# Optimization experiments

Measured on AMD Instinct MI355X. Metric: run time of the kernel, lower is better.

The kernel has to match this reference:

```python
import jax, jax.numpy as jnp
import numpy as np

DIM = 256
NUM_HEADS = 8
HEAD_DIM = DIM // NUM_HEADS  # 32 (MQA: k/v projected to a single head)
RPE_DIM = 128
P = 10            # cpb table resolution per axis ('bilinear_4_10')
MAX_VALUE = 4.0
LOG_SCALE = 512.0
LOG2_8 = 3.0      # np.log2(8)


def _trilinear_sample(table, grid):
    """torch F.grid_sample 3D, mode='bilinear', padding_mode='zeros', align_corners=True.
    table: [C, D, H, W]; grid: [M, 3] with (x,y,z) in [-1,1] -> returns [C, M]."""
    C, D, H, W = table.shape
    x = (grid[:, 0] + 1.0) * 0.5 * (W - 1)
    y = (grid[:, 1] + 1.0) * 0.5 * (H - 1)
    z = (grid[:, 2] + 1.0) * 0.5 * (D - 1)
    x0f, y0f, z0f = jnp.floor(x), jnp.floor(y), jnp.floor(z)
    wx1, wy1, wz1 = x - x0f, y - y0f, z - z0f
    wx0, wy0, wz0 = 1.0 - wx1, 1.0 - wy1, 1.0 - wz1
    x0 = x0f.astype(jnp.int32); x1 = x0 + 1
    y0 = y0f.astype(jnp.int32); y1 = y0 + 1
    z0 = z0f.astype(jnp.int32); z1 = z0 + 1

    def corner(iz, iy, ix, w):
        inb = (iz >= 0) & (iz < D) & (iy >= 0) & (iy < H) & (ix >= 0) & (ix < W)
        v = table[:, jnp.clip(iz, 0, D - 1), jnp.clip(iy, 0, H - 1), jnp.clip(ix, 0, W - 1)]
        return v * jnp.where(inb, w, 0.0)[None, :]

    return (corner(z0, y0, x0, wz0 * wy0 * wx0) + corner(z0, y0, x1, wz0 * wy0 * wx1)
          + corner(z0, y1, x0, wz0 * wy1 * wx0) + corner(z0, y1, x1, wz0 * wy1 * wx1)
          + corner(z1, y0, x0, wz1 * wy0 * wx0) + corner(z1, y0, x1, wz1 * wy0 * wx1)
          + corner(z1, y1, x0, wz1 * wy1 * wx0) + corner(z1, y1, x1, wz1 * wy1 * wx1))


def setup_inputs() -> dict:
    rng = jax.random.key(0)
    ks = jax.random.split(rng, 12)
    B, nQ, nK = 2, 256, 2048
    s = 0.02
    return {
        "query": jax.random.normal(ks[0], (nQ, B, DIM), jnp.float32),
        "key": jax.random.normal(ks[1], (nK, B, DIM), jnp.float32),
        "reference_point": jax.random.normal(ks[2], (B, nQ, 8, 3), jnp.float32),
        "reference_angle": jax.random.normal(ks[3], (B, nQ), jnp.float32),
        "xyz_vol": jax.random.normal(ks[4], (B, nK, 3), jnp.float32),
        "q_w": jax.random.normal(ks[5], (DIM, DIM), jnp.float32) * s,
        "q_b": jnp.zeros((DIM,), jnp.float32),
        "k_w": jax.random.normal(ks[6], (DIM, HEAD_DIM), jnp.float32) * s,
        "k_b": jnp.zeros((HEAD_DIM,), jnp.float32),
        "v_w": jax.random.normal(ks[7], (DIM, HEAD_DIM), jnp.float32) * s,
        "v_b": jnp.zeros((HEAD_DIM,), jnp.float32),
        "proj_w": jax.random.normal(ks[8], (DIM, DIM), jnp.float32) * s,
        "proj_b": jnp.zeros((DIM,), jnp.float32),
        "cpb_w1": jax.random.normal(ks[9], (8, 3, RPE_DIM), jnp.float32) * s,
        "cpb_b1": jnp.zeros((8, RPE_DIM), jnp.float32),
        "cpb_w2": jax.random.normal(ks[10], (8, RPE_DIM, NUM_HEADS), jnp.float32) * s,
    }


def reference(query, key, reference_point, reference_angle, xyz_vol,
              q_w, q_b, k_w, k_b, v_w, v_b, proj_w, proj_b,
              cpb_w1, cpb_b1, cpb_w2):
    B, nQ = reference_point.shape[:2]
    nK = xyz_vol.shape[1]
    q_in = jnp.transpose(query, (1, 0, 2))  # [B, nQ, DIM]
    k_in = jnp.transpose(key, (1, 0, 2))    # [B, nK, DIM]

    # CPB MLP evaluated on the fixed coords table -> per-corner tables [8, NUM_HEADS, P, P, P]
    lin = jnp.linspace(-MAX_VALUE, MAX_VALUE, P, dtype=jnp.float32)
    coords = jnp.stack(jnp.meshgrid(lin, lin, lin, indexing='ij'), axis=-1)  # [P,P,P,3]
    hid = jax.nn.relu(jnp.einsum('pqrc,icd->ipqrd', coords, cpb_w1) + cpb_b1[:, None, None, None, :])
    tables = jnp.einsum('ipqrd,idh->ihpqr', hid, cpb_w2)

    # log-scaled relative deltas for all 8 corners (angle_type=='' -> no rotation branch)
    d = reference_point[:, :, None, :, :] - xyz_vol[:, None, :, None, :]  # [B,nQ,nK,8,3]
    d = jnp.sign(d) * jnp.log2(jnp.abs(d) * LOG_SCALE + 1.0) / LOG2_8 / MAX_VALUE
    grids = jnp.moveaxis(d, 3, 0).reshape(8, -1, 3)  # [8, B*nQ*nK, 3]

    sampled = jax.vmap(_trilinear_sample)(tables, grids)  # [8, NUM_HEADS, M]
    rpe = jnp.transpose(sampled.sum(0).reshape(NUM_HEADS, B, nQ, nK), (1, 0, 2, 3))  # [B,H,nQ,nK]

    scale = HEAD_DIM ** -0.5
    q = (q_in @ q_w + q_b).reshape(B, nQ, NUM_HEADS, HEAD_DIM)
    k = k_in @ k_w + k_b  # [B, nK, HEAD_DIM] (single shared KV head)
    v = k_in @ v_w + v_b
    attn = jnp.einsum('bqhd,bkd->bhqk', q * scale, k) + rpe
    attn = jax.nn.softmax(attn, axis=-1)
    x = jnp.einsum('bhqk,bkd->bqhd', attn, v).reshape(B, nQ, DIM)
    x = x @ proj_w + proj_b
    return jnp.transpose(x, (1, 0, 2)), attn
```

## Files before the change

### kernel.cpp

```cpp
#include <hip/hip_runtime.h>
#include <hip/hip_bf16.h>
#include <cstdint>

#define NQ 256
#define NK 2048
#define BB 2
#define SCALE 0.17677669529663687f

#define TB_OFF 0u
#define QP_OFF 128000u
#define KT_OFF 652288u
#define VP_OFF 1176576u
#define X_OFF  1700864u

typedef unsigned short u16;
typedef _Float16 h16;
union U16x8 { uint4 u; h16 h[8]; };

__global__ __launch_bounds__(512) void k_prep(const float* __restrict__ query,
                                              const float* __restrict__ key,
                                              const float* __restrict__ qw,
                                              const float* __restrict__ qb,
                                              const float* __restrict__ kw,
                                              const float* __restrict__ kb,
                                              const float* __restrict__ vw,
                                              const float* __restrict__ vb,
                                              const float* __restrict__ w1g,
                                              const float* __restrict__ b1g,
                                              const float* __restrict__ w2g,
                                              u16* __restrict__ tb,
                                              float* __restrict__ qp,
                                              float* __restrict__ kpT,
                                              float* __restrict__ vp) {
  __shared__ __align__(16) char smraw[16 * 257 * 4];
  int bid = blockIdx.x, t = threadIdx.x;

  if (bid < 256) {
    float (*rows)[257] = (float(*)[257])smraw;
    int b = bid >> 7, kc = bid & 127;
    for (int idx = t; idx < 4096; idx += 512) {
      int r = idx >> 8, m = idx & 255;
      rows[r][m] = key[((kc * 16 + r) * BB + b) * 256 + m];
    }
    __syncthreads();
    int ks = t >> 5, d = t & 31;
    float a = kb[d], av = vb[d];
    #pragma unroll 4
    for (int m = 0; m < 256; ++m) {
      float rv = rows[ks][m];
      a  = fmaf(rv, kw[m * 32 + d], a);
      av = fmaf(rv, vw[m * 32 + d], av);
    }
    int k = kc * 16 + ks;
    vp[(b * NK + k) * 32 + d] = av;
    __syncthreads();
    float* f1 = (float*)smraw;
    f1[d * 16 + ks] = a;
    __syncthreads();
    int dd = t >> 4, kk = t & 15;
    kpT[(b * 32 + dd) * NK + kc * 16 + kk] = f1[dd * 16 + kk];
  } else if (bid < 320) {
    float (*rows)[257] = (float(*)[257])smraw;
    int qg = bid - 256;
    for (int idx = t; idx < 2048; idx += 512) {
      int r = idx >> 8, m = idx & 255;
      int g = qg * 8 + r, b = g >> 8, q = g & 255;
      rows[r][m] = query[(q * BB + b) * 256 + m];
    }
    __syncthreads();
    int r = t >> 6, c0 = (t & 63) * 4;
    int g = qg * 8 + r;
    float4 acc = *(const float4*)&qb[c0];
    #pragma unroll 4
    for (int m = 0; m < 256; ++m) {
      float rv = rows[r][m];
      float4 w4 = *(const float4*)&qw[m * 256 + c0];
      acc.x = fmaf(rv, w4.x, acc.x); acc.y = fmaf(rv, w4.y, acc.y);
      acc.z = fmaf(rv, w4.z, acc.z); acc.w = fmaf(rv, w4.w, acc.w);
    }
    float4 o; o.x = acc.x * SCALE; o.y = acc.y * SCALE; o.z = acc.z * SCALE; o.w = acc.w * SCALE;
    *(float4*)&qp[g * 256 + c0] = o;
  } else {
    float* w1 = (float*)smraw;
    float* b1 = w1 + 384;
    float* w2 = b1 + 128;
    int i = bid - 320;
    for (int idx = t; idx < 384; idx += 512) w1[idx] = w1g[i * 384 + idx];
    if (t < 128) b1[t] = b1g[i * 128 + t];
    for (int idx = t; idx < 1024; idx += 512) w2[idx] = w2g[i * 1024 + idx];
    __syncthreads();
    for (int cell = t; cell < 1000; cell += 512) {
      int z = cell / 100, y = (cell / 10) % 10, x = cell % 10;
      const float step = 8.0f / 9.0f;
      float cz = -4.f + z * step, cy = -4.f + y * step, cx = -4.f + x * step;
      float o0 = 0, o1 = 0, o2 = 0, o3 = 0, o4 = 0, o5 = 0, o6 = 0, o7 = 0;
      for (int d = 0; d < 128; ++d) {
        float h = fmaxf(fmaf(cz, w1[d], fmaf(cy, w1[128 + d], fmaf(cx, w1[256 + d], b1[d]))), 0.f);
        const float* w2r = &w2[d * 8];
        o0 = fmaf(h, w2r[0], o0); o1 = fmaf(h, w2r[1], o1);
        o2 = fmaf(h, w2r[2], o2); o3 = fmaf(h, w2r[3], o3);
        o4 = fmaf(h, w2r[4], o4); o5 = fmaf(h, w2r[5], o5);
        o6 = fmaf(h, w2r[6], o6); o7 = fmaf(h, w2r[7], o7);
      }
      U16x8 R;
      R.h[0] = (h16)o0; R.h[1] = (h16)o1; R.h[2] = (h16)o2; R.h[3] = (h16)o3;
      R.h[4] = (h16)o4; R.h[5] = (h16)o5; R.h[6] = (h16)o6; R.h[7] = (h16)o7;
      *(uint4*)&tb[i * 8000 + cell * 8] = R.u;
    }
  }
}

struct Axis { int o0, o1; float w0, w1; };

static __device__ __forceinline__ Axis axis_setup(float dv, int stride) {
  float g = copysignf(__log2f(fmaf(fabsf(dv), 512.f, 1.f)) * (1.f / 12.f), dv);
  float p = fmaf(g, 4.5f, 4.5f);
  float f = floorf(p);
  int i0 = (int)f;
  float w1v = p - f;
  float w0v = 1.f - w1v;
  Axis a;
  a.w0 = ((unsigned)i0 <= 9u) ? w0v : 0.f;
  a.w1 = ((unsigned)(i0 + 1) <= 9u) ? w1v : 0.f;
  int c0 = min(max(i0, 0), 9);
  int c1 = min(max(i0 + 1, 0), 9);
  a.o0 = c0 * stride;
  a.o1 = c1 * stride;
  return a;
}

#define DO_CORNER(CU, W, J) do { float ww = (W); \
  acc[0][J] = fmaf((float)(CU).h[0], ww, acc[0][J]); \
  acc[1][J] = fmaf((float)(CU).h[1], ww, acc[1][J]); \
  acc[2][J] = fmaf((float)(CU).h[2], ww, acc[2][J]); \
  acc[3][J] = fmaf((float)(CU).h[3], ww, acc[3][J]); \
  acc[4][J] = fmaf((float)(CU).h[4], ww, acc[4][J]); \
  acc[5][J] = fmaf((float)(CU).h[5], ww, acc[5][J]); \
  acc[6][J] = fmaf((float)(CU).h[6], ww, acc[6][J]); \
  acc[7][J] = fmaf((float)(CU).h[7], ww, acc[7][J]); } while (0)

__global__ __launch_bounds__(1024, 4) void k_main(const u16* __restrict__ tbw,
                                                  const float* __restrict__ qp,
                                                  const float* __restrict__ kpT,
                                                  const float* __restrict__ xyz,
                                                  const float* __restrict__ refp,
                                                  float* __restrict__ attn) {
  __shared__ __align__(16) u16 tb[64000];
  __shared__ __align__(16) float qrow[2][256];
  __shared__ __align__(16) float rp[2][24];
  __shared__ __align__(16) float red[2][64];
  int t = threadIdx.x;
  int b = blockIdx.x >> 7, qc = blockIdx.x & 127;
  for (int idx = t; idx < 8000; idx += 1024)
    ((uint4*)tb)[idx] = ((const uint4*)tbw)[idx];
  if (t < 128) {
    int qh2 = t >> 6, c = t & 63;
    ((float4*)qrow[qh2])[c] = ((const float4*)(qp + (b * 256 + qc * 2 + qh2) * 256))[c];
  } else if (t < 140) {
    int idx = t - 128;
    int qh2 = idx / 6, c = idx % 6;
    ((float4*)rp[qh2])[c] = ((const float4*)(refp + (b * 256 + qc * 2 + qh2) * 24))[c];
  }
  __syncthreads();

  int wv = t >> 6, l = t & 63;
  int qh = wv >> 3, wvl = wv & 7;
  int q = qc * 2 + qh;
  int k0 = wvl * 256 + l * 4;
  float acc[8][4] = {};

  const float* kT = kpT + b * (32 * NK);
  #pragma unroll 2
  for (int dq = 0; dq < 8; ++dq) {
    const float* kp0 = kT + (dq * 4) * NK + k0;
    float4 kv0 = *(const float4*)(kp0);
    float4 kv1 = *(const float4*)(kp0 + NK);
    float4 kv2 = *(const float4*)(kp0 + 2 * NK);
    float4 kv3 = *(const float4*)(kp0 + 3 * NK);
    #pragma unroll
    for (int h = 0; h < 8; ++h) {
      float4 qv = *(const float4*)&qrow[qh][h * 32 + dq * 4];
      acc[h][0] = fmaf(qv.x, kv0.x, fmaf(qv.y, kv1.x, fmaf(qv.z, kv2.x, fmaf(qv.w, kv3.x, acc[h][0]))));
      acc[h][1] = fmaf(qv.x, kv0.y, fmaf(qv.y, kv1.y, fmaf(qv.z, kv2.y, fmaf(qv.w, kv3.y, acc[h][1]))));
      acc[h][2] = fmaf(qv.x, kv0.z, fmaf(qv.y, kv1.z, fmaf(qv.z, kv2.z, fmaf(qv.w, kv3.z, acc[h][2]))));
      acc[h][3] = fmaf(qv.x, kv0.w, fmaf(qv.y, kv1.w, fmaf(qv.z, kv2.w, fmaf(qv.w, kv3.w, acc[h][3]))));
    }
  }

  {
    const float* xp = xyz + (size_t)(b * NK + k0) * 3;
    float4 X0 = *(const float4*)(xp);
    float4 X1 = *(const float4*)(xp + 4);
    float4 X2 = *(const float4*)(xp + 8);
    float xv[4] = { X0.x, X0.w, X1.z, X2.y };
    float yv[4] = { X0.y, X1.x, X1.w, X2.z };
    float zv[4] = { X0.z, X1.y, X2.x, X2.w };
    #pragma unroll 1
    for (int i = 0; i < 8; ++i) {
      float rx = rp[qh][i * 3 + 0];
      float ry = rp[qh][i * 3 + 1];
      float rz = rp[qh][i * 3 + 2];
      const u16* tp = tb + i * 8000;
      #pragma unroll
      for (int j = 0; j < 4; ++j) {
        Axis ax = axis_setup(rx - xv[j], 8);
        Axis ay = axis_setup(ry - yv[j], 80);
        Axis az = axis_setup(rz - zv[j], 800);
        float w00 = az.w0 * ay.w0, w01 = az.w0 * ay.w1;
        float w10 = az.w1 * ay.w0, w11 = az.w1 * ay.w1;
        U16x8 u;
        u.u = *(const uint4*)(tp + az.o0 + ay.o0 + ax.o0); DO_CORNER(u, w00 * ax.w0, j);
        u.u = *(const uint4*)(tp + az.o0 + ay.o0 + ax.o1); DO_CORNER(u, w00 * ax.w1, j);
        u.u = *(const uint4*)(tp + az.o0 + ay.o1 + ax.o0); DO_CORNER(u, w01 * ax.w0, j);
        u.u = *(const uint4*)(tp + az.o0 + ay.o1 + ax.o1); DO_CORNER(u, w01 * ax.w1, j);
        u.u = *(const uint4*)(tp + az.o1 + ay.o0 + ax.o0); DO_CORNER(u, w10 * ax.w0, j);
        u.u = *(const uint4*)(tp + az.o1 + ay.o0 + ax.o1); DO_CORNER(u, w10 * ax.w1, j);
        u.u = *(const uint4*)(tp + az.o1 + ay.o1 + ax.o0); DO_CORNER(u, w11 * ax.w0, j);
        u.u = *(const uint4*)(tp + az.o1 + ay.o1 + ax.o1); DO_CORNER(u, w11 * ax.w1, j);
      }
    }
  }

  float mx[8];
  #pragma unroll
  for (int h = 0; h < 8; ++h) {
    float m = fmaxf(fmaxf(acc[h][0], acc[h][1]), fmaxf(acc[h][2], acc[h][3]));
    #pragma unroll
    for (int off = 32; off >= 1; off >>= 1) m = fmaxf(m, __shfl_xor(m, off, 64));
    mx[h] = m;
  }
  if (l == 0) {
    #pragma unroll
    for (int h = 0; h < 8; ++h) red[qh][h * 8 + wvl] = mx[h];
  }
  __syncthreads();
  #pragma unroll
  for (int h = 0; h < 8; ++h) {
    float4 r0 = *(const float4*)&red[qh][h * 8];
    float4 r1 = *(const float4*)&red[qh][h * 8 + 4];
    mx[h] = fmaxf(fmaxf(fmaxf(r0.x, r0.y), fmaxf(r0.z, r0.w)),
                  fmaxf(fmaxf(r1.x, r1.y), fmaxf(r1.z, r1.w)));
  }
  __syncthreads();
  float sm[8];
  #pragma unroll
  for (int h = 0; h < 8; ++h) {
    acc[h][0] = __expf(acc[h][0] - mx[h]);
    acc[h][1] = __expf(acc[h][1] - mx[h]);
    acc[h][2] = __expf(acc[h][2] - mx[h]);
    acc[h][3] = __expf(acc[h][3] - mx[h]);
    float s = (acc[h][0] + acc[h][1]) + (acc[h][2] + acc[h][3]);
    #pragma unroll
    for (int off = 32; off >= 1; off >>= 1) s += __shfl_xor(s, off, 64);
    sm[h] = s;
  }
  if (l == 0) {
    #pragma unroll
    for (int h = 0; h < 8; ++h) red[qh][h * 8 + wvl] = sm[h];
  }
  __syncthreads();
  #pragma unroll
  for (int h = 0; h < 8; ++h) {
    float4 r0 = *(const float4*)&red[qh][h * 8];
    float4 r1 = *(const float4*)&red[qh][h * 8 + 4];
    float s = ((r0.x + r0.y) + (r0.z + r0.w)) + ((r1.x + r1.y) + (r1.z + r1.w));
    float inv = 1.f / s;
    float4 pv;
    pv.x = acc[h][0] * inv; pv.y = acc[h][1] * inv;
    pv.z = acc[h][2] * inv; pv.w = acc[h][3] * inv;
    *(float4*)&attn[((b * 8 + h) * 256 + q) * 2048 + k0] = pv;
  }
}

#define AV_ACC(A, s, v) { (A).x = fmaf((s), (v).x, (A).x); (A).y = fmaf((s), (v).y, (A).y); \
                          (A).z = fmaf((s), (v).z, (A).z); (A).w = fmaf((s), (v).w, (A).w); }

__global__ __launch_bounds__(256) void k_av(const float* __restrict__ attn,
                                            const float* __restrict__ vp,
                                            float* __restrict__ xpart) {
  int bid = blockIdx.x;
  int kh = bid & 7, qt = (bid >> 3) & 3, h = (bid >> 5) & 7, b = bid >> 8;
  int t = threadIdx.x;
  int qr = t >> 3, dq = t & 7;
  int q0 = qt * 64 + qr * 2;
  const float* ar0 = attn + ((size_t)((b * 8 + h) * 256 + q0)) * 2048 + kh * 256;
  const float* ar1 = ar0 + 2048;
  const float* vbase = vp + ((size_t)(b * NK + kh * 256)) * 32 + dq * 4;
  float4 A0 = {0, 0, 0, 0}, A1 = {0, 0, 0, 0};
  #pragma unroll 4
  for (int k = 0; k < 256; k += 4) {
    float4 a0 = *(const float4*)&ar0[k];
    float4 a1 = *(const float4*)&ar1[k];
    float4 v0 = *(const float4*)&vbase[(k + 0) * 32];
    float4 v1 = *(const float4*)&vbase[(k + 1) * 32];
    float4 v2 = *(const float4*)&vbase[(k + 2) * 32];
    float4 v3 = *(const float4*)&vbase[(k + 3) * 32];
    AV_ACC(A0, a0.x, v0) AV_ACC(A0, a0.y, v1) AV_ACC(A0, a0.z, v2) AV_ACC(A0, a0.w, v3)
    AV_ACC(A1, a1.x, v0) AV_ACC(A1, a1.y, v1) AV_ACC(A1, a1.z, v2) AV_ACC(A1, a1.w, v3)
  }
  int o = (b * 256 + q0) * 256 + h * 32 + dq * 4;
  *(float4*)&xpart[kh * 131072 + o] = A0;
  *(float4*)&xpart[kh * 131072 + o + 256] = A1;
}

__global__ __launch_bounds__(256) void k_out(const float* __restrict__ xpart,
                                             const float* __restrict__ pw,
                                             const float* __restrict__ pb,
                                             float* __restrict__ out) {
  __shared__ float xr[4][257];
  int b = blockIdx.x >> 6, qc = blockIdx.x & 63, t = threadIdx.x;
  for (int idx = t; idx < 1024; idx += 256) {
    int r = idx >> 8, m = idx & 255;
    int q = qc * 4 + r;
    int o = (b * 256 + q) * 256 + m;
    float s = 0.f;
    #pragma unroll
    for (int kh = 0; kh < 8; ++kh) s += xpart[kh * 131072 + o];
    xr[r][m] = s;
  }
  __syncthreads();
  int r = t >> 6, c0 = (t & 63) * 4;
  float4 a = *(const float4*)&pb[c0];
  #pragma unroll 4
  for (int m = 0; m < 256; ++m) {
    float rv = xr[r][m];
    float4 w4 = *(const float4*)&pw[m * 256 + c0];
    a.x = fmaf(rv, w4.x, a.x); a.y = fmaf(rv, w4.y, a.y);
    a.z = fmaf(rv, w4.z, a.z); a.w = fmaf(rv, w4.w, a.w);
  }
  int q = qc * 4 + r;
  *(float4*)&out[(q * BB + b) * 256 + c0] = a;
}

extern "C" void kernel_launch(void* const* d_in, const int* in_sizes, int n_in,
                              void* d_out, int out_size, void* d_ws, size_t ws_size,
                              hipStream_t stream) {
  const float* query = (const float*)d_in[0];
  const float* key   = (const float*)d_in[1];
  const float* refp  = (const float*)d_in[2];
  const float* xyz   = (const float*)d_in[4];
  const float* qw    = (const float*)d_in[5];
  const float* qb    = (const float*)d_in[6];
  const float* kw    = (const float*)d_in[7];
  const float* kb    = (const float*)d_in[8];
  const float* vw    = (const float*)d_in[9];
  const float* vb    = (const float*)d_in[10];
  const float* pw    = (const float*)d_in[11];
  const float* pb    = (const float*)d_in[12];
  const float* w1    = (const float*)d_in[13];
  const float* b1    = (const float*)d_in[14];
  const float* w2    = (const float*)d_in[15];

  char* ws = (char*)d_ws;
  u16*   tb    = (u16*)(ws + TB_OFF);
  float* qp    = (float*)(ws + QP_OFF);
  float* kpT   = (float*)(ws + KT_OFF);
  float* vp    = (float*)(ws + VP_OFF);
  float* xpart = (float*)(ws + X_OFF);
  float* out  = (float*)d_out;
  float* attn = out + 131072;

  hipLaunchKernelGGL(k_prep, dim3(328), dim3(512),  0, stream,
                     query, key, qw, qb, kw, kb, vw, vb, w1, b1, w2, tb, qp, kpT, vp);
  hipLaunchKernelGGL(k_main, dim3(256), dim3(1024), 0, stream, tb, qp, kpT, xyz, refp, attn);
  hipLaunchKernelGGL(k_av,   dim3(512), dim3(256),  0, stream, attn, vp, xpart);
  hipLaunchKernelGGL(k_out,  dim3(128), dim3(256),  0, stream, xpart, pw, pb, out);
}
```

Baseline: 217.6 us.

## Fuse attention-times-V and output projection into main attention kernel

```diff
diff --git a/kernel.cpp b/kernel.cpp
--- a/kernel.cpp
+++ b/kernel.cpp
@@ -11,7 +11,6 @@
 #define QP_OFF 128000u
 #define KT_OFF 652288u
 #define VP_OFF 1176576u
-#define X_OFF  1700864u
 
 typedef unsigned short u16;
 typedef _Float16 h16;
@@ -84,12 +83,14 @@
     float* w1 = (float*)smraw;
     float* b1 = w1 + 384;
     float* w2 = b1 + 128;
-    int i = bid - 320;
+    int ib = bid - 320;
+    int i = ib >> 2, cc = ib & 3;
     for (int idx = t; idx < 384; idx += 512) w1[idx] = w1g[i * 384 + idx];
     if (t < 128) b1[t] = b1g[i * 128 + t];
     for (int idx = t; idx < 1024; idx += 512) w2[idx] = w2g[i * 1024 + idx];
     __syncthreads();
-    for (int cell = t; cell < 1000; cell += 512) {
+    if (t < 250) {
+      int cell = cc * 250 + t;
       int z = cell / 100, y = (cell / 10) % 10, x = cell % 10;
       const float step = 8.0f / 9.0f;
       float cz = -4.f + z * step, cy = -4.f + y * step, cx = -4.f + x * step;
@@ -139,16 +140,24 @@
   acc[6][J] = fmaf((float)(CU).h[6], ww, acc[6][J]); \
   acc[7][J] = fmaf((float)(CU).h[7], ww, acc[7][J]); } while (0)
 
-__global__ __launch_bounds__(1024, 4) void k_main(const u16* __restrict__ tbw,
+__global__ __launch_bounds__(1024, 4) void k_mega(const u16* __restrict__ tbw,
                                                   const float* __restrict__ qp,
                                                   const float* __restrict__ kpT,
                                                   const float* __restrict__ xyz,
                                                   const float* __restrict__ refp,
-                                                  float* __restrict__ attn) {
-  __shared__ __align__(16) u16 tb[64000];
+                                                  const float* __restrict__ vp,
+                                                  const float* __restrict__ pw,
+                                                  const float* __restrict__ pb,
+                                                  float* __restrict__ attn,
+                                                  float* __restrict__ out) {
+  __shared__ __align__(16) char un[131072];
+  __shared__ __align__(16) float red4[2][8][8][32];
   __shared__ __align__(16) float qrow[2][256];
   __shared__ __align__(16) float rp[2][24];
   __shared__ __align__(16) float red[2][64];
+  u16* tb = (u16*)un;
+  float* p = (float*)un;
+
   int t = threadIdx.x;
   int b = blockIdx.x >> 7, qc = blockIdx.x & 127;
   for (int idx = t; idx < 8000; idx += 1024)
@@ -165,7 +174,6 @@
 
   int wv = t >> 6, l = t & 63;
   int qh = wv >> 3, wvl = wv & 7;
-  int q = qc * 2 + qh;
   int k0 = wvl * 256 + l * 4;
   float acc[8][4] = {};
 
@@ -268,68 +276,85 @@
     float4 pv;
     pv.x = acc[h][0] * inv; pv.y = acc[h][1] * inv;
     pv.z = acc[h][2] * inv; pv.w = acc[h][3] * inv;
-    *(float4*)&attn[((b * 8 + h) * 256 + q) * 2048 + k0] = pv;
-  }
-}
-
-#define AV_ACC(A, s, v) { (A).x = fmaf((s), (v).x, (A).x); (A).y = fmaf((s), (v).y, (A).y); \
-                          (A).z = fmaf((s), (v).z, (A).z); (A).w = fmaf((s), (v).w, (A).w); }
-
-__global__ __launch_bounds__(256) void k_av(const float* __restrict__ attn,
-                                            const float* __restrict__ vp,
-                                            float* __restrict__ xpart) {
-  int bid = blockIdx.x;
-  int kh = bid & 7, qt = (bid >> 3) & 3, h = (bid >> 5) & 7, b = bid >> 8;
-  int t = threadIdx.x;
-  int qr = t >> 3, dq = t & 7;
-  int q0 = qt * 64 + qr * 2;
-  const float* ar0 = attn + ((size_t)((b * 8 + h) * 256 + q0)) * 2048 + kh * 256;
-  const float* ar1 = ar0 + 2048;
-  const float* vbase = vp + ((size_t)(b * NK + kh * 256)) * 32 + dq * 4;
-  float4 A0 = {0, 0, 0, 0}, A1 = {0, 0, 0, 0};
-  #pragma unroll 4
-  for (int k = 0; k < 256; k += 4) {
-    float4 a0 = *(const float4*)&ar0[k];
-    float4 a1 = *(const float4*)&ar1[k];
-    float4 v0 = *(const float4*)&vbase[(k + 0) * 32];
-    float4 v1 = *(const float4*)&vbase[(k + 1) * 32];
-    float4 v2 = *(const float4*)&vbase[(k + 2) * 32];
-    float4 v3 = *(const float4*)&vbase[(k + 3) * 32];
-    AV_ACC(A0, a0.x, v0) AV_ACC(A0, a0.y, v1) AV_ACC(A0, a0.z, v2) AV_ACC(A0, a0.w, v3)
-    AV_ACC(A1, a1.x, v0) AV_ACC(A1, a1.y, v1) AV_ACC(A1, a1.z, v2) AV_ACC(A1, a1.w, v3)
-  }
-  int o = (b * 256 + q0) * 256 + h * 32 + dq * 4;
-  *(float4*)&xpart[kh * 131072 + o] = A0;
-  *(float4*)&xpart[kh * 131072 + o + 256] = A1;
-}
-
-__global__ __launch_bounds__(256) void k_out(const float* __restrict__ xpart,
-                                             const float* __restrict__ pw,
-                                             const float* __restrict__ pb,
-                                             float* __restrict__ out) {
-  __shared__ float xr[4][257];
-  int b = blockIdx.x >> 6, qc = blockIdx.x & 63, t = threadIdx.x;
-  for (int idx = t; idx < 1024; idx += 256) {
-    int r = idx >> 8, m = idx & 255;
-    int q = qc * 4 + r;
-    int o = (b * 256 + q) * 256 + m;
+    *(float4*)&p[(qh * 8 + h) * 2048 + k0] = pv;
+  }
+  __syncthreads();
+
+  #pragma unroll
+  for (int c = 0; c < 8; ++c) {
+    int flat = (c * 1024 + t) * 4;
+    int qh2 = flat >> 14, h2 = (flat >> 11) & 7, kk = flat & 2047;
+    float4 pv4 = *(const float4*)&p[(qh2 * 8 + h2) * 2048 + kk];
+    *(float4*)&attn[((size_t)((b * 8 + h2) * 256 + (qc * 2 + qh2))) * 2048 + kk] = pv4;
+  }
+
+  {
+    int ch = wv >> 1, pqh = wv & 1;
+    int ks2 = l >> 3, dq = l & 7;
+    float a2[8][4] = {};
+    const float* vbase = vp + ((size_t)(b * NK + ch * 256)) * 32 + dq * 4;
+    const float* prow = p + pqh * 16384 + ch * 256;
+    #pragma unroll 2
+    for (int kk = 0; kk < 32; ++kk) {
+      int ko = kk * 8 + ks2;
+      float4 v4 = *(const float4*)&vbase[ko * 32];
+      #pragma unroll
+      for (int h = 0; h < 8; ++h) {
+        float pvv = prow[h * 2048 + ko];
+        a2[h][0] = fmaf(pvv, v4.x, a2[h][0]);
+        a2[h][1] = fmaf(pvv, v4.y, a2[h][1]);
+        a2[h][2] = fmaf(pvv, v4.z, a2[h][2]);
+        a2[h][3] = fmaf(pvv, v4.w, a2[h][3]);
+      }
+    }
+    #pragma unroll
+    for (int off = 8; off <= 32; off <<= 1) {
+      #pragma unroll
+      for (int h = 0; h < 8; ++h) {
+        a2[h][0] += __shfl_xor(a2[h][0], off, 64);
+        a2[h][1] += __shfl_xor(a2[h][1], off, 64);
+        a2[h][2] += __shfl_xor(a2[h][2], off, 64);
+        a2[h][3] += __shfl_xor(a2[h][3], off, 64);
+      }
+    }
+    if (ks2 == 0) {
+      #pragma unroll
+      for (int h = 0; h < 8; ++h) {
+        float4 w4; w4.x = a2[h][0]; w4.y = a2[h][1]; w4.z = a2[h][2]; w4.w = a2[h][3];
+        *(float4*)&red4[pqh][ch][h][dq * 4] = w4;
+      }
+    }
+  }
+  __syncthreads();
+  if (t < 512) {
+    int pqh = t >> 8, m = t & 255;
+    int h = m >> 5, d = m & 31;
     float s = 0.f;
     #pragma unroll
-    for (int kh = 0; kh < 8; ++kh) s += xpart[kh * 131072 + o];
-    xr[r][m] = s;
-  }
-  __syncthreads();
-  int r = t >> 6, c0 = (t & 63) * 4;
-  float4 a = *(const float4*)&pb[c0];
-  #pragma unroll 4
-  for (int m = 0; m < 256; ++m) {
-    float rv = xr[r][m];
-    float4 w4 = *(const float4*)&pw[m * 256 + c0];
-    a.x = fmaf(rv, w4.x, a.x); a.y = fmaf(rv, w4.y, a.y);
-    a.z = fmaf(rv, w4.z, a.z); a.w = fmaf(rv, w4.w, a.w);
-  }
-  int q = qc * 4 + r;
-  *(float4*)&out[(q * BB + b) * 256 + c0] = a;
+    for (int ch = 0; ch < 8; ++ch) s += red4[pqh][ch][h][d];
+    qrow[pqh][m] = s;
+  }
+  __syncthreads();
+
+  {
+    float* scratch = (float*)red4;
+    int c = t & 255, half = (t >> 8) & 1, pqh = t >> 9;
+    int m0 = half * 128;
+    float a = 0.f;
+    #pragma unroll 4
+    for (int m = 0; m < 128; ++m) {
+      a = fmaf(qrow[pqh][m0 + m], pw[(m0 + m) * 256 + c], a);
+    }
+    scratch[(pqh * 2 + half) * 256 + c] = a;
+  }
+  __syncthreads();
+  if (t < 512) {
+    float* scratch = (float*)red4;
+    int pqh = t >> 8, c = t & 255;
+    float v = scratch[(pqh * 2) * 256 + c] + scratch[(pqh * 2 + 1) * 256 + c] + pb[c];
+    int q = qc * 2 + pqh;
+    out[(q * BB + b) * 256 + c] = v;
+  }
 }
 
 extern "C" void kernel_launch(void* const* d_in, const int* in_sizes, int n_in,
@@ -352,17 +377,15 @@
   const float* w2    = (const float*)d_in[15];
 
   char* ws = (char*)d_ws;
-  u16*   tb    = (u16*)(ws + TB_OFF);
-  float* qp    = (float*)(ws + QP_OFF);
-  float* kpT   = (float*)(ws + KT_OFF);
-  float* vp    = (float*)(ws + VP_OFF);
-  float* xpart = (float*)(ws + X_OFF);
+  u16*   tb  = (u16*)(ws + TB_OFF);
+  float* qp  = (float*)(ws + QP_OFF);
+  float* kpT = (float*)(ws + KT_OFF);
+  float* vp  = (float*)(ws + VP_OFF);
   float* out  = (float*)d_out;
   float* attn = out + 131072;
 
-  hipLaunchKernelGGL(k_prep, dim3(328), dim3(512),  0, stream,
+  hipLaunchKernelGGL(k_prep, dim3(352), dim3(512),  0, stream,
                      query, key, qw, qb, kw, kb, vw, vb, w1, b1, w2, tb, qp, kpT, vp);
-  hipLaunchKernelGGL(k_main, dim3(256), dim3(1024), 0, stream, tb, qp, kpT, xyz, refp, attn);
-  hipLaunchKernelGGL(k_av,   dim3(512), dim3(256),  0, stream, attn, vp, xpart);
-  hipLaunchKernelGGL(k_out,  dim3(128), dim3(256),  0, stream, xpart, pw, pb, out);
+  hipLaunchKernelGGL(k_mega, dim3(256), dim3(1024), 0, stream,
+                     tb, qp, kpT, xyz, refp, vp, pw, pb, attn, out);
 }
```

New measurement: 193.6 us. 1.12x faster.
